# Kernel optimization log

Measured on AMD Instinct MI355X. Metric: run time of the kernel, lower is better.

## Reference

```python
import jax, jax.numpy as jnp
import numpy as np

T, IN_DIM, MEM_DIM = 8192, 2048, 2048


def setup_inputs() -> dict:
    key = jax.random.key(0)
    ks = jax.random.split(key, 7)
    s = 0.02
    return {
        "inputs": jax.random.normal(ks[0], (T, IN_DIM), dtype=jnp.float32),
        "Wx": jax.random.normal(ks[1], (5 * MEM_DIM, IN_DIM), dtype=jnp.float32) * s,
        "bx": jax.random.normal(ks[2], (5 * MEM_DIM,), dtype=jnp.float32) * s,
        "Wh": jax.random.normal(ks[3], (4 * MEM_DIM, MEM_DIM), dtype=jnp.float32) * s,
        "bh": jax.random.normal(ks[4], (4 * MEM_DIM,), dtype=jnp.float32) * s,
        "Wm": jax.random.normal(ks[5], (MEM_DIM, MEM_DIM), dtype=jnp.float32) * s,
        "bm": jax.random.normal(ks[6], (MEM_DIM,), dtype=jnp.float32) * s,
    }


def reference(inputs, Wx, bx, Wh, bh, Wm, bm):
    # Precompute input projections for all timesteps in one GEMM: (T, 5M)
    xg = inputs @ Wx.T + bx

    def step(carry, x5):
        c, h = carry  # each (mem_dim,)
        ix, ox, zx, fx, ux = jnp.split(x5, 5)
        gh = Wh @ h + bh
        ih, oh, zh, fh = jnp.split(gh, 4)
        i = jax.nn.sigmoid(ix + ih)
        o = jax.nn.sigmoid(ox + oh)
        f = jax.nn.sigmoid(fx + fh)
        z = jax.nn.sigmoid(zx + zh)
        u = jnp.tanh(ux + Wm @ (z * jnp.tanh(c)) + bm)
        c_new = i * u + f * c
        h_new = o * jnp.tanh(c_new)  # use_o=True
        return (c_new, h_new), None

    init = (jnp.zeros((MEM_DIM,), inputs.dtype), jnp.zeros((MEM_DIM,), inputs.dtype))
    (c_T, h_T), _ = jax.lax.scan(step, init, xg)
    return h_T[None, :]  # (1, mem_dim), matching torch forward's returned h
```

## Files before the change

### kernel.cpp

```cpp
#include <hip/hip_runtime.h>
#include <cstdio>
#include <cstdint>
#include <cstddef>


#define T_STEPS 8192
#define MEM     2048
#define NG5     10240
#define NBLK    256
#define NTHR    512
#define RCOPY   8

static constexpr size_t XG_BYTES  = (size_t)T_STEPS * NG5 * 2;
static constexpr size_t HREP_OFF  = XG_BYTES;
static constexpr size_t REP_BYTES = (size_t)RCOPY * NBLK * 64;
static constexpr size_t AREP_OFF  = HREP_OFF + REP_BYTES;
static constexpr size_t WS_NEEDED = AREP_OFF + REP_BYTES;

__device__ __forceinline__ float bf2f(unsigned short u) {
  return __uint_as_float(((unsigned int)u) << 16);
}
__device__ __forceinline__ unsigned short f2bf(float f) {
  unsigned int u = __float_as_uint(f);
  u += 0x7FFFu + ((u >> 16) & 1u);
  return (unsigned short)(u >> 16);
}
__device__ __forceinline__ float sigmoidf_(float x) {
  return 1.0f / (1.0f + __expf(-x));
}
__device__ __forceinline__ float tanhf_(float x) {
  x = fminf(fmaxf(x, -15.0f), 15.0f);
  float e = __expf(2.0f * x);
  return (e - 1.0f) / (e + 1.0f);
}

__device__ __forceinline__ void store_i_cc(int* p, int v) {
  asm volatile("global_store_dword %0, %1, off sc0 sc1"
               :: "v"(p), "v"(v) : "memory");
}
__device__ __forceinline__ int4 load4_cc(const float* p) {
  int4 v;
  asm volatile("global_load_dwordx4 %0, %1, off sc0 sc1\n\t"
               "s_waitcnt vmcnt(0)"
               : "=v"(v) : "v"(p) : "memory");
  return v;
}

__global__ void fplstm_init(int* rep) {
  const int tid = threadIdx.x;
  const int n = 2 * RCOPY * NBLK * 16;
  for (int i = tid; i < n; i += 256) rep[i] = 0;
}

__global__ __launch_bounds__(256, 2) void fplstm_gemm(
    const float* __restrict__ A, const float* __restrict__ W,
    const float* __restrict__ bx, unsigned short* __restrict__ xg)
{
  __shared__ float As[16][132];
  __shared__ float Bs[16][144];
  const int tid = threadIdx.x;
  const int bn = blockIdx.x;
  const int bm = blockIdx.y;
  const int tx = tid & 15, ty = tid >> 4;
  const int lrow = tid >> 1;
  const int kh   = (tid & 1) * 8;
  const float* Ap = A + (size_t)(bm * 128 + lrow) * 2048 + kh;
  const float* Wp = W + (size_t)(bn * 128 + lrow) * 2048 + kh;
  const int bmap = lrow + 4 * (lrow >> 5);
  const int bb   = 8 * tx + 4 * (tx >> 2);

  float acc[8][8];
#pragma unroll
  for (int i = 0; i < 8; ++i)
#pragma unroll
    for (int j = 0; j < 8; ++j) acc[i][j] = 0.0f;

  for (int k0 = 0; k0 < 2048; k0 += 16) {
    float4 a0 = *(const float4*)(Ap + k0);
    float4 a1 = *(const float4*)(Ap + k0 + 4);
    float4 b0 = *(const float4*)(Wp + k0);
    float4 b1 = *(const float4*)(Wp + k0 + 4);
    __syncthreads();
    As[kh+0][lrow] = a0.x; As[kh+1][lrow] = a0.y; As[kh+2][lrow] = a0.z; As[kh+3][lrow] = a0.w;
    As[kh+4][lrow] = a1.x; As[kh+5][lrow] = a1.y; As[kh+6][lrow] = a1.z; As[kh+7][lrow] = a1.w;
    Bs[kh+0][bmap] = b0.x; Bs[kh+1][bmap] = b0.y; Bs[kh+2][bmap] = b0.z; Bs[kh+3][bmap] = b0.w;
    Bs[kh+4][bmap] = b1.x; Bs[kh+5][bmap] = b1.y; Bs[kh+6][bmap] = b1.z; Bs[kh+7][bmap] = b1.w;
    __syncthreads();
#pragma unroll
    for (int k = 0; k < 16; ++k) {
      float4 x0 = *(const float4*)(&As[k][8 * ty]);
      float4 x1 = *(const float4*)(&As[k][8 * ty + 4]);
      float4 y0 = *(const float4*)(&Bs[k][bb]);
      float4 y1 = *(const float4*)(&Bs[k][bb + 4]);
      float xa[8] = {x0.x, x0.y, x0.z, x0.w, x1.x, x1.y, x1.z, x1.w};
      float yb[8] = {y0.x, y0.y, y0.z, y0.w, y1.x, y1.y, y1.z, y1.w};
#pragma unroll
      for (int i = 0; i < 8; ++i)
#pragma unroll
        for (int j = 0; j < 8; ++j)
          acc[i][j] = fmaf(xa[i], yb[j], acc[i][j]);
    }
  }

  float bxa[8];
  {
    float4 q0 = *(const float4*)(bx + bn * 128 + 8 * tx);
    float4 q1 = *(const float4*)(bx + bn * 128 + 8 * tx + 4);
    bxa[0]=q0.x; bxa[1]=q0.y; bxa[2]=q0.z; bxa[3]=q0.w;
    bxa[4]=q1.x; bxa[5]=q1.y; bxa[6]=q1.z; bxa[7]=q1.w;
  }
#pragma unroll
  for (int i = 0; i < 8; ++i) {
    const size_t row = (size_t)(bm * 128 + 8 * ty + i);
    unsigned short t8[8];
#pragma unroll
    for (int j = 0; j < 8; ++j) t8[j] = f2bf(acc[i][j] + bxa[j]);
    unsigned short* p = xg + row * NG5 + bn * 128 + 8 * tx;
    *(ushort4*)(p)     = make_ushort4(t8[0], t8[1], t8[2], t8[3]);
    *(ushort4*)(p + 4) = make_ushort4(t8[4], t8[5], t8[6], t8[7]);
  }
}

__global__ __launch_bounds__(NTHR, 2) void fplstm_recur(
    const unsigned short* __restrict__ xg,
    float* hrep, float* arep,
    const float* __restrict__ Wh, const float* __restrict__ bh,
    const float* __restrict__ Wm, const float* __restrict__ bm,
    float* __restrict__ out)
{
  const int tid  = threadIdx.x;
  const int b    = blockIdx.x;
  const int w    = tid >> 6;
  const int lane = tid & 63;
  const int rg   = w & 3;
  const int hf   = w >> 2;
  const int colbase = 1024 * hf + 4 * lane;

  float whr[8][16];
#pragma unroll
  for (int r = 0; r < 8; ++r) {
    const float* wp = Wh + (size_t)(rg * MEM + 8 * b + r) * MEM + colbase;
#pragma unroll
    for (int k = 0; k < 4; ++k) {
      float4 v = *(const float4*)(wp + 256 * k);
      whr[r][4*k+0] = v.x; whr[r][4*k+1] = v.y; whr[r][4*k+2] = v.z; whr[r][4*k+3] = v.w;
    }
  }
  float wmr[2][16];
#pragma unroll
  for (int r = 0; r < 2; ++r) {
    const float* wp = Wm + (size_t)(8 * b + 2 * rg + r) * MEM + colbase;
#pragma unroll
    for (int k = 0; k < 4; ++k) {
      float4 v = *(const float4*)(wp + 256 * k);
      wmr[r][4*k+0] = v.x; wmr[r][4*k+1] = v.y; wmr[r][4*k+2] = v.z; wmr[r][4*k+3] = v.w;
    }
  }

  float bhv0 = 0, bhv1 = 0, bhv2 = 0, bhv3 = 0, bmv = 0;
  if (tid < 8) {
    bhv0 = bh[0 * MEM + 8 * b + tid];
    bhv1 = bh[1 * MEM + 8 * b + tid];
    bhv2 = bh[2 * MEM + 8 * b + tid];
    bhv3 = bh[3 * MEM + 8 * b + tid];
    bmv  = bm[8 * b + tid];
  }

  __shared__ float hs[MEM];
  __shared__ float redL[8][8];
  __shared__ float ghL[32];
  __shared__ float redM[8][2];

  const int copy  = b & 7;
  const int line  = 32 * w + (lane >> 1);
  const int half  = lane & 1;
  const float* hl = hrep + (size_t)(copy * NBLK + line) * 16 + 4 * half;
  const float* al = arep + (size_t)(copy * NBLK + line) * 16 + 4 * half;

  int* a_dst = (int*)(arep + (size_t)((lane >> 3) * NBLK + b) * 16) + (lane & 7);
  int* h_dst = (int*)(hrep + (size_t)((lane >> 3) * NBLK + b) * 16) + (lane & 7);

  float c_e = 0.0f, h_last = 0.0f;

  for (int t = 0; t < T_STEPS; ++t) {
    float xv0 = 0, xv1 = 0, xv2 = 0, xv3 = 0, xv4 = 0;
    if (tid < 8) {
      const unsigned short* xp = xg + (size_t)t * NG5 + 8 * b + tid;
      xv0 = bf2f(xp[0]);
      xv1 = bf2f(xp[1 * MEM]);
      xv2 = bf2f(xp[2 * MEM]);
      xv3 = bf2f(xp[3 * MEM]);
      xv4 = bf2f(xp[4 * MEM]);
    }

    {
      const int e2 = (2 * t) & 3;
      int4 v;
      for (;;) {
        v = load4_cc(hl);
        const int bad = ((v.x ^ e2) | (v.y ^ e2) | (v.z ^ e2) | (v.w ^ e2)) & 3;
        if (__all(bad == 0)) break;
      }
      *(int4*)&hs[8 * line + 4 * half] = v;
    }
    __syncthreads();

    float hreg[16];
#pragma unroll
    for (int k = 0; k < 4; ++k) {
      float4 v = *(const float4*)&hs[colbase + 256 * k];
      hreg[4*k+0] = v.x; hreg[4*k+1] = v.y; hreg[4*k+2] = v.z; hreg[4*k+3] = v.w;
    }
    float acc[8];
#pragma unroll
    for (int r = 0; r < 8; ++r) {
      float s = 0.0f;
#pragma unroll
      for (int j = 0; j < 16; ++j) s = fmaf(whr[r][j], hreg[j], s);
      acc[r] = s;
    }
    float v4[4];
    {
      const int b0 = lane & 1;
#pragma unroll
      for (int i = 0; i < 4; ++i) {
        float sent = b0 ? acc[i] : acc[4 + i];
        float got  = __shfl_xor(sent, 1, 64);
        v4[i] = (b0 ? acc[4 + i] : acc[i]) + got;
      }
    }
    float v2[2];
    {
      const int b1 = (lane >> 1) & 1;
#pragma unroll
      for (int i = 0; i < 2; ++i) {
        float sent = b1 ? v4[i] : v4[2 + i];
        float got  = __shfl_xor(sent, 2, 64);
        v2[i] = (b1 ? v4[2 + i] : v4[i]) + got;
      }
    }
    float v1r;
    {
      const int b2 = (lane >> 2) & 1;
      float sent = b2 ? v2[0] : v2[1];
      float got  = __shfl_xor(sent, 4, 64);
      v1r = (b2 ? v2[1] : v2[0]) + got;
    }
    v1r += __shfl_xor(v1r, 8, 64);
    v1r += __shfl_xor(v1r, 16, 64);
    v1r += __shfl_xor(v1r, 32, 64);
    if (lane < 8) {
      const int r = 4 * (lane & 1) + 2 * ((lane >> 1) & 1) + ((lane >> 2) & 1);
      redL[w][r] = v1r;
    }
    __syncthreads();

    float g_i = 0, g_o = 0, g_fc = 0, a_e = 0;
    if (w == 0) {
      if (tid < 32)
        ghL[tid] = redL[tid >> 3][tid & 7] + redL[(tid >> 3) + 4][tid & 7];
      if (tid < 8) {
        float gi = sigmoidf_(xv0 + ghL[tid]      + bhv0);
        float go = sigmoidf_(xv1 + ghL[8 + tid]  + bhv1);
        float gz = sigmoidf_(xv2 + ghL[16 + tid] + bhv2);
        float gf = sigmoidf_(xv3 + ghL[24 + tid] + bhv3);
        a_e = gz * tanhf_(c_e);
        g_i = gi; g_o = go; g_fc = gf * c_e;
      }
      float av = __shfl(a_e, lane & 7, 64);
      store_i_cc(a_dst, (__float_as_int(av) & ~3) | ((2 * t + 1) & 3));
    }

    {
      const int e2 = (2 * t + 1) & 3;
      int4 v;
      for (;;) {
        v = load4_cc(al);
        const int bad = ((v.x ^ e2) | (v.y ^ e2) | (v.z ^ e2) | (v.w ^ e2)) & 3;
        if (__all(bad == 0)) break;
      }
      *(int4*)&hs[8 * line + 4 * half] = v;
    }
    __syncthreads();

    float areg[16];
#pragma unroll
    for (int k = 0; k < 4; ++k) {
      float4 v = *(const float4*)&hs[colbase + 256 * k];
      areg[4*k+0] = v.x; areg[4*k+1] = v.y; areg[4*k+2] = v.z; areg[4*k+3] = v.w;
    }
    float am0 = 0.0f, am1 = 0.0f;
#pragma unroll
    for (int j = 0; j < 16; ++j) am0 = fmaf(wmr[0][j], areg[j], am0);
#pragma unroll
    for (int j = 0; j < 16; ++j) am1 = fmaf(wmr[1][j], areg[j], am1);
    {
      float sent = (lane & 1) ? am0 : am1;
      float got  = __shfl_xor(sent, 1, 64);
      float vv = ((lane & 1) ? am1 : am0) + got;
      vv += __shfl_xor(vv, 2, 64);
      vv += __shfl_xor(vv, 4, 64);
      vv += __shfl_xor(vv, 8, 64);
      vv += __shfl_xor(vv, 16, 64);
      vv += __shfl_xor(vv, 32, 64);
      if (lane < 2) redM[w][lane] = vv;
    }
    __syncthreads();

    if (w == 0) {
      if (tid < 8) {
        float mg = redM[tid >> 1][tid & 1] + redM[(tid >> 1) + 4][tid & 1];
        float u  = tanhf_(xv4 + mg + bmv);
        c_e    = fmaf(g_i, u, g_fc);
        h_last = g_o * tanhf_(c_e);
      }
      float hv = __shfl(h_last, lane & 7, 64);
      store_i_cc(h_dst, (__float_as_int(hv) & ~3) | ((2 * t + 2) & 3));
    }
  }

  if (tid < 8) out[8 * b + tid] = h_last;
}

extern "C" void kernel_launch(void* const* d_in, const int* in_sizes, int n_in,
                              void* d_out, int out_size, void* d_ws, size_t ws_size,
                              hipStream_t stream) {
  const float* inputs = (const float*)d_in[0];
  const float* Wx     = (const float*)d_in[1];
  const float* bx     = (const float*)d_in[2];
  const float* Wh     = (const float*)d_in[3];
  const float* bh     = (const float*)d_in[4];
  const float* Wm     = (const float*)d_in[5];
  const float* bm     = (const float*)d_in[6];
  float* out = (float*)d_out;
  char* ws = (char*)d_ws;

  if (ws_size < WS_NEEDED) {
    fprintf(stderr, "FPLSTM: ws_size %zu < needed %zu -- cannot run\n",
            ws_size, (size_t)WS_NEEDED);
    return;
  }

  unsigned short* xg = (unsigned short*)ws;
  float* hrep = (float*)(ws + HREP_OFF);
  float* arep = (float*)(ws + AREP_OFF);

  fplstm_init<<<1, 256, 0, stream>>>((int*)hrep);
  fplstm_gemm<<<dim3(80, 64), 256, 0, stream>>>(inputs, Wx, bx, xg);

  void* args[] = {(void*)&xg, (void*)&hrep, (void*)&arep,
                  (void*)&Wh, (void*)&bh, (void*)&Wm, (void*)&bm, (void*)&out};
  hipError_t e = hipLaunchCooperativeKernel((void*)fplstm_recur, dim3(NBLK),
                                            dim3(NTHR), args, 0, stream);
  if (e != hipSuccess) {
    fprintf(stderr, "FPLSTM: coop launch failed (%d), plain launch\n", (int)e);
    fplstm_recur<<<dim3(NBLK), dim3(NTHR), 0, stream>>>(
        xg, hrep, arep, Wh, bh, Wm, bm, out);
  }
}
```

Baseline: 42.85 ms.

## Distribute per-element gate math across warps and drop a block barrier per step

Each of the 8 warps now owns one of the block's 8 state elements. Every warp computes its own i/o/f gates, its full Wm row dot product and its cell update, instead of funnelling all element math through warp 0. The z-gate warp waits on a shared-memory flag rather than a full __syncthreads before publishing the a-vector, and double shared buffers (hsA/hsB) let the next phase start without another barrier. The goal is to shorten the serial critical path of each recurrent step. In exchange there is a spin-wait on shared memory, redundant transcendental work across lanes, and more registers for the Wm row.

Measured after the change: 55.44 ms. 1.29x slower.

```diff
diff --git a/kernel.cpp b/kernel.cpp
--- a/kernel.cpp
+++ b/kernel.cpp
@@ -44,6 +44,15 @@
                "s_waitcnt vmcnt(0)"
                : "=v"(v) : "v"(p) : "memory");
   return v;
+}
+__device__ __forceinline__ bool quad_ok(const int4 v, const int e2) {
+  return ((((v.x ^ e2) | (v.y ^ e2) | (v.z ^ e2) | (v.w ^ e2)) & 3) == 0);
+}
+__device__ __forceinline__ int4 poll_quad(const float* p, const int e2) {
+  for (;;) {
+    int4 v = load4_cc(p);
+    if (__all(quad_ok(v, e2))) return v;
+  }
 }
 
 __global__ void fplstm_init(int* rep) {
@@ -135,6 +144,8 @@
   const int rg   = w & 3;
   const int hf   = w >> 2;
   const int colbase = 1024 * hf + 4 * lane;
+  const int j7   = lane & 7;
+  const int rperm = ((j7 & 1) << 2) | (j7 & 2) | ((j7 >> 2) & 1);
 
   float whr[8][16];
 #pragma unroll
@@ -146,30 +157,29 @@
       whr[r][4*k+0] = v.x; whr[r][4*k+1] = v.y; whr[r][4*k+2] = v.z; whr[r][4*k+3] = v.w;
     }
   }
-  float wmr[2][16];
-#pragma unroll
-  for (int r = 0; r < 2; ++r) {
-    const float* wp = Wm + (size_t)(8 * b + 2 * rg + r) * MEM + colbase;
-#pragma unroll
-    for (int k = 0; k < 4; ++k) {
+  float wm32[32];
+  {
+    const float* wp = Wm + (size_t)(8 * b + w) * MEM + 4 * lane;
+#pragma unroll
+    for (int k = 0; k < 8; ++k) {
       float4 v = *(const float4*)(wp + 256 * k);
-      wmr[r][4*k+0] = v.x; wmr[r][4*k+1] = v.y; wmr[r][4*k+2] = v.z; wmr[r][4*k+3] = v.w;
-    }
-  }
-
-  float bhv0 = 0, bhv1 = 0, bhv2 = 0, bhv3 = 0, bmv = 0;
-  if (tid < 8) {
-    bhv0 = bh[0 * MEM + 8 * b + tid];
-    bhv1 = bh[1 * MEM + 8 * b + tid];
-    bhv2 = bh[2 * MEM + 8 * b + tid];
-    bhv3 = bh[3 * MEM + 8 * b + tid];
-    bmv  = bm[8 * b + tid];
-  }
-
-  __shared__ float hs[MEM];
+      wm32[4*k+0] = v.x; wm32[4*k+1] = v.y; wm32[4*k+2] = v.z; wm32[4*k+3] = v.w;
+    }
+  }
+  const float bhi = bh[0 * MEM + 8 * b + w];
+  const float bho = bh[1 * MEM + 8 * b + w];
+  const float bhf = bh[3 * MEM + 8 * b + w];
+  const float bmw = bm[8 * b + w];
+  const float bhz = bh[2 * MEM + 8 * b + rperm];
+
+  __shared__ float hsA[MEM];
+  __shared__ float hsB[MEM];
   __shared__ float redL[8][8];
-  __shared__ float ghL[32];
-  __shared__ float redM[8][2];
+  __shared__ float tcL[8];
+  __shared__ int   zflag;
+
+  if (tid == 0) zflag = 0;
+  if (tid < 8) tcL[tid] = 0.0f;
 
   const int copy  = b & 7;
   const int line  = 32 * w + (lane >> 1);
@@ -177,38 +187,30 @@
   const float* hl = hrep + (size_t)(copy * NBLK + line) * 16 + 4 * half;
   const float* al = arep + (size_t)(copy * NBLK + line) * 16 + 4 * half;
 
-  int* a_dst = (int*)(arep + (size_t)((lane >> 3) * NBLK + b) * 16) + (lane & 7);
-  int* h_dst = (int*)(hrep + (size_t)((lane >> 3) * NBLK + b) * 16) + (lane & 7);
-
-  float c_e = 0.0f, h_last = 0.0f;
+  int* a_pub = (int*)arep + ((size_t)((lane >> 3) * NBLK + b) * 16 + j7);
+  int* h_pub = (int*)hrep + ((size_t)(lane * NBLK + b) * 16 + w);
+
+  float c_w = 0.0f, h_keep = 0.0f;
 
   for (int t = 0; t < T_STEPS; ++t) {
-    float xv0 = 0, xv1 = 0, xv2 = 0, xv3 = 0, xv4 = 0;
-    if (tid < 8) {
-      const unsigned short* xp = xg + (size_t)t * NG5 + 8 * b + tid;
-      xv0 = bf2f(xp[0]);
-      xv1 = bf2f(xp[1 * MEM]);
-      xv2 = bf2f(xp[2 * MEM]);
-      xv3 = bf2f(xp[3 * MEM]);
-      xv4 = bf2f(xp[4 * MEM]);
-    }
-
-    {
-      const int e2 = (2 * t) & 3;
-      int4 v;
-      for (;;) {
-        v = load4_cc(hl);
-        const int bad = ((v.x ^ e2) | (v.y ^ e2) | (v.z ^ e2) | (v.w ^ e2)) & 3;
-        if (__all(bad == 0)) break;
-      }
-      *(int4*)&hs[8 * line + 4 * half] = v;
+    const unsigned short* xrow = xg + (size_t)t * NG5 + 8 * b;
+    const float xvi = bf2f(xrow[0 * MEM + w]);
+    const float xvo = bf2f(xrow[1 * MEM + w]);
+    const float xvf = bf2f(xrow[3 * MEM + w]);
+    const float xvu = bf2f(xrow[4 * MEM + w]);
+    float xvz = 0.0f;
+    if (w == 2) xvz = bf2f(xrow[2 * MEM + rperm]);
+
+    {
+      int4 v = poll_quad(hl, (2 * t) & 3);
+      *(int4*)&hsA[8 * line + 4 * half] = v;
     }
     __syncthreads();
 
     float hreg[16];
 #pragma unroll
     for (int k = 0; k < 4; ++k) {
-      float4 v = *(const float4*)&hs[colbase + 256 * k];
+      float4 v = *(const float4*)&hsA[colbase + 256 * k];
       hreg[4*k+0] = v.x; hreg[4*k+1] = v.y; hreg[4*k+2] = v.z; hreg[4*k+3] = v.w;
     }
     float acc[8];
@@ -249,77 +251,64 @@
     v1r += __shfl_xor(v1r, 8, 64);
     v1r += __shfl_xor(v1r, 16, 64);
     v1r += __shfl_xor(v1r, 32, 64);
-    if (lane < 8) {
-      const int r = 4 * (lane & 1) + 2 * ((lane >> 1) & 1) + ((lane >> 2) & 1);
-      redL[w][r] = v1r;
-    }
-    __syncthreads();
-
-    float g_i = 0, g_o = 0, g_fc = 0, a_e = 0;
-    if (w == 0) {
-      if (tid < 32)
-        ghL[tid] = redL[tid >> 3][tid & 7] + redL[(tid >> 3) + 4][tid & 7];
-      if (tid < 8) {
-        float gi = sigmoidf_(xv0 + ghL[tid]      + bhv0);
-        float go = sigmoidf_(xv1 + ghL[8 + tid]  + bhv1);
-        float gz = sigmoidf_(xv2 + ghL[16 + tid] + bhv2);
-        float gf = sigmoidf_(xv3 + ghL[24 + tid] + bhv3);
-        a_e = gz * tanhf_(c_e);
-        g_i = gi; g_o = go; g_fc = gf * c_e;
+
+    if (w == 2) {
+      while (*(volatile int*)&zflag < t + 1) { }
+      __threadfence_block();
+      const float zh = v1r + redL[6][rperm];
+      const float z  = sigmoidf_(xvz + zh + bhz);
+      const float ap = z * tcL[rperm];
+      const float av = __shfl(ap, rperm, 64);
+      store_i_cc(a_pub, (__float_as_int(av) & ~3) | (int)((2 * t + 1) & 3));
+    } else {
+      if (lane < 8) redL[w][rperm] = v1r;
+      if (w == 6) {
+        __threadfence_block();
+        if (lane == 0) *(volatile int*)&zflag = t + 1;
       }
-      float av = __shfl(a_e, lane & 7, 64);
-      store_i_cc(a_dst, (__float_as_int(av) & ~3) | ((2 * t + 1) & 3));
-    }
-
-    {
-      const int e2 = (2 * t + 1) & 3;
-      int4 v;
-      for (;;) {
-        v = load4_cc(al);
-        const int bad = ((v.x ^ e2) | (v.y ^ e2) | (v.z ^ e2) | (v.w ^ e2)) & 3;
-        if (__all(bad == 0)) break;
-      }
-      *(int4*)&hs[8 * line + 4 * half] = v;
-    }
-    __syncthreads();
-
-    float areg[16];
-#pragma unroll
-    for (int k = 0; k < 4; ++k) {
-      float4 v = *(const float4*)&hs[colbase + 256 * k];
-      areg[4*k+0] = v.x; areg[4*k+1] = v.y; areg[4*k+2] = v.z; areg[4*k+3] = v.w;
-    }
-    float am0 = 0.0f, am1 = 0.0f;
-#pragma unroll
-    for (int j = 0; j < 16; ++j) am0 = fmaf(wmr[0][j], areg[j], am0);
-#pragma unroll
-    for (int j = 0; j < 16; ++j) am1 = fmaf(wmr[1][j], areg[j], am1);
-    {
-      float sent = (lane & 1) ? am0 : am1;
-      float got  = __shfl_xor(sent, 1, 64);
-      float vv = ((lane & 1) ? am1 : am0) + got;
-      vv += __shfl_xor(vv, 2, 64);
-      vv += __shfl_xor(vv, 4, 64);
-      vv += __shfl_xor(vv, 8, 64);
-      vv += __shfl_xor(vv, 16, 64);
-      vv += __shfl_xor(vv, 32, 64);
-      if (lane < 2) redM[w][lane] = vv;
-    }
-    __syncthreads();
-
-    if (w == 0) {
-      if (tid < 8) {
-        float mg = redM[tid >> 1][tid & 1] + redM[(tid >> 1) + 4][tid & 1];
-        float u  = tanhf_(xv4 + mg + bmv);
-        c_e    = fmaf(g_i, u, g_fc);
-        h_last = g_o * tanhf_(c_e);
-      }
-      float hv = __shfl(h_last, lane & 7, 64);
-      store_i_cc(h_dst, (__float_as_int(hv) & ~3) | ((2 * t + 2) & 3));
-    }
-  }
-
-  if (tid < 8) out[8 * b + tid] = h_last;
+    }
+    __syncthreads();
+
+    const float gi = sigmoidf_(xvi + redL[0][w] + redL[4][w] + bhi);
+    const float go = sigmoidf_(xvo + redL[1][w] + redL[5][w] + bho);
+    const float gf = sigmoidf_(xvf + redL[3][w] + redL[7][w] + bhf);
+    const float fc = gf * c_w;
+
+    {
+      int4 v = poll_quad(al, (2 * t + 1) & 3);
+      *(int4*)&hsB[8 * line + 4 * half] = v;
+    }
+    __syncthreads();
+
+    float s0 = 0.0f, s1 = 0.0f, s2 = 0.0f, s3 = 0.0f;
+#pragma unroll
+    for (int k = 0; k < 8; ++k) {
+      float4 q = *(const float4*)&hsB[4 * lane + 256 * k];
+      s0 = fmaf(wm32[4*k+0], q.x, s0);
+      s1 = fmaf(wm32[4*k+1], q.y, s1);
+      s2 = fmaf(wm32[4*k+2], q.z, s2);
+      s3 = fmaf(wm32[4*k+3], q.w, s3);
+    }
+    float mg = (s0 + s1) + (s2 + s3);
+    mg += __shfl_xor(mg, 1, 64);
+    mg += __shfl_xor(mg, 2, 64);
+    mg += __shfl_xor(mg, 4, 64);
+    mg += __shfl_xor(mg, 8, 64);
+    mg += __shfl_xor(mg, 16, 64);
+    mg += __shfl_xor(mg, 32, 64);
+
+    const float uu  = tanhf_(xvu + mg + bmw);
+    const float cn  = fmaf(gi, uu, fc);
+    const float tch = tanhf_(cn);
+    const float hv  = go * tch;
+    c_w = cn;
+    if (lane == 0) tcL[w] = tch;
+    if (lane < 8)
+      store_i_cc(h_pub, (__float_as_int(hv) & ~3) | (int)((2 * t + 2) & 3));
+    h_keep = hv;
+  }
+
+  if (lane == 0) out[8 * b + w] = h_keep;
 }
 
 extern "C" void kernel_launch(void* const* d_in, const int* in_sizes, int n_in,
```

## Pack broadcast replicas densely and interleave xg gates per block

Applied to the files above, without the earlier changes.

The h/a broadcast replica buffers were padded to 64-byte lines with only 32 bytes used per block. They are now packed contiguously, so each wave polls 1 KB of consecutive memory per replica copy. The GEMM epilogue writes xg in a block-interleaved layout so each recurrent block's five gate values for a timestep sit within 80 contiguous bytes instead of five strided locations. The goal is fewer cache lines touched in the latency-bound per-step polling and gate loads. The trade-off is more writers sharing each cache line, which may add coherence contention.

After: 42.30 ms. About the same (-1.3%).

```diff
diff --git a/kernel.cpp b/kernel.cpp
--- a/kernel.cpp
+++ b/kernel.cpp
@@ -13,7 +13,7 @@
 
 static constexpr size_t XG_BYTES  = (size_t)T_STEPS * NG5 * 2;
 static constexpr size_t HREP_OFF  = XG_BYTES;
-static constexpr size_t REP_BYTES = (size_t)RCOPY * NBLK * 64;
+static constexpr size_t REP_BYTES = (size_t)RCOPY * NBLK * 32;
 static constexpr size_t AREP_OFF  = HREP_OFF + REP_BYTES;
 static constexpr size_t WS_NEEDED = AREP_OFF + REP_BYTES;
 
@@ -45,10 +45,19 @@
                : "=v"(v) : "v"(p) : "memory");
   return v;
 }
+__device__ __forceinline__ bool quad_ok(const int4 v, const int e2) {
+  return ((((v.x ^ e2) | (v.y ^ e2) | (v.z ^ e2) | (v.w ^ e2)) & 3) == 0);
+}
+__device__ __forceinline__ int4 poll_quad(const float* p, const int e2) {
+  for (;;) {
+    int4 v = load4_cc(p);
+    if (__all(quad_ok(v, e2))) return v;
+  }
+}
 
 __global__ void fplstm_init(int* rep) {
   const int tid = threadIdx.x;
-  const int n = 2 * RCOPY * NBLK * 16;
+  const int n = 2 * RCOPY * NBLK * 8;
   for (int i = tid; i < n; i += 256) rep[i] = 0;
 }
 
@@ -109,13 +118,17 @@
     bxa[0]=q0.x; bxa[1]=q0.y; bxa[2]=q0.z; bxa[3]=q0.w;
     bxa[4]=q1.x; bxa[5]=q1.y; bxa[6]=q1.z; bxa[7]=q1.w;
   }
+  const int n5 = bn * 128 + 8 * tx;
+  const int g  = n5 >> 11;
+  const int el = n5 & 2047;
+  const size_t po = (size_t)(el >> 3) * 40 + g * 8;
 #pragma unroll
   for (int i = 0; i < 8; ++i) {
     const size_t row = (size_t)(bm * 128 + 8 * ty + i);
     unsigned short t8[8];
 #pragma unroll
     for (int j = 0; j < 8; ++j) t8[j] = f2bf(acc[i][j] + bxa[j]);
-    unsigned short* p = xg + row * NG5 + bn * 128 + 8 * tx;
+    unsigned short* p = xg + row * NG5 + po;
     *(ushort4*)(p)     = make_ushort4(t8[0], t8[1], t8[2], t8[3]);
     *(ushort4*)(p + 4) = make_ushort4(t8[4], t8[5], t8[6], t8[7]);
   }
@@ -171,37 +184,30 @@
   __shared__ float ghL[32];
   __shared__ float redM[8][2];
 
-  const int copy  = b & 7;
-  const int line  = 32 * w + (lane >> 1);
-  const int half  = lane & 1;
-  const float* hl = hrep + (size_t)(copy * NBLK + line) * 16 + 4 * half;
-  const float* al = arep + (size_t)(copy * NBLK + line) * 16 + 4 * half;
-
-  int* a_dst = (int*)(arep + (size_t)((lane >> 3) * NBLK + b) * 16) + (lane & 7);
-  int* h_dst = (int*)(hrep + (size_t)((lane >> 3) * NBLK + b) * 16) + (lane & 7);
+  const int copy = b & 7;
+  const int soff = 256 * w + 4 * lane;
+  const float* hl = hrep + (size_t)copy * 2048 + soff;
+  const float* al = arep + (size_t)copy * 2048 + soff;
+
+  int* a_dst = (int*)arep + ((size_t)(lane >> 3) * 2048 + b * 8 + (lane & 7));
+  int* h_dst = (int*)hrep + ((size_t)(lane >> 3) * 2048 + b * 8 + (lane & 7));
 
   float c_e = 0.0f, h_last = 0.0f;
 
   for (int t = 0; t < T_STEPS; ++t) {
     float xv0 = 0, xv1 = 0, xv2 = 0, xv3 = 0, xv4 = 0;
     if (tid < 8) {
-      const unsigned short* xp = xg + (size_t)t * NG5 + 8 * b + tid;
+      const unsigned short* xp = xg + (size_t)t * NG5 + 40 * b + tid;
       xv0 = bf2f(xp[0]);
-      xv1 = bf2f(xp[1 * MEM]);
-      xv2 = bf2f(xp[2 * MEM]);
-      xv3 = bf2f(xp[3 * MEM]);
-      xv4 = bf2f(xp[4 * MEM]);
-    }
-
-    {
-      const int e2 = (2 * t) & 3;
-      int4 v;
-      for (;;) {
-        v = load4_cc(hl);
-        const int bad = ((v.x ^ e2) | (v.y ^ e2) | (v.z ^ e2) | (v.w ^ e2)) & 3;
-        if (__all(bad == 0)) break;
-      }
-      *(int4*)&hs[8 * line + 4 * half] = v;
+      xv1 = bf2f(xp[8]);
+      xv2 = bf2f(xp[16]);
+      xv3 = bf2f(xp[24]);
+      xv4 = bf2f(xp[32]);
+    }
+
+    {
+      int4 v = poll_quad(hl, (2 * t) & 3);
+      *(int4*)&hs[soff] = v;
     }
     __syncthreads();
 
@@ -268,18 +274,12 @@
         g_i = gi; g_o = go; g_fc = gf * c_e;
       }
       float av = __shfl(a_e, lane & 7, 64);
-      store_i_cc(a_dst, (__float_as_int(av) & ~3) | ((2 * t + 1) & 3));
-    }
-
-    {
-      const int e2 = (2 * t + 1) & 3;
-      int4 v;
-      for (;;) {
-        v = load4_cc(al);
-        const int bad = ((v.x ^ e2) | (v.y ^ e2) | (v.z ^ e2) | (v.w ^ e2)) & 3;
-        if (__all(bad == 0)) break;
-      }
-      *(int4*)&hs[8 * line + 4 * half] = v;
+      store_i_cc(a_dst, (__float_as_int(av) & ~3) | (int)((2 * t + 1) & 3));
+    }
+
+    {
+      int4 v = poll_quad(al, (2 * t + 1) & 3);
+      *(int4*)&hs[soff] = v;
     }
     __syncthreads();
 
@@ -315,7 +315,7 @@
         h_last = g_o * tanhf_(c_e);
       }
       float hv = __shfl(h_last, lane & 7, 64);
-      store_i_cc(h_dst, (__float_as_int(hv) & ~3) | ((2 * t + 2) & 3));
+      store_i_cc(h_dst, (__float_as_int(hv) & ~3) | (int)((2 * t + 2) & 3));
     }
   }
 
```
